# Kernel optimization log

Hardware: AMD Instinct MI355X
Metric: run time of the kernel (lower is better)

Reference implementation:

```python
import jax, jax.numpy as jnp
import numpy as np

OUT_FEATURES = 4096
IN_FEATURES = 4096
BLOCK_DIM = 16
K = 64
N_BLOCKS = OUT_FEATURES * IN_FEATURES // BLOCK_DIM  # 1,048,576


def setup_inputs() -> dict:
    key = jax.random.key(0)
    k1, k2, k3, k4, k5, k6 = jax.random.split(key, 6)
    x = jax.random.normal(k1, (8192, IN_FEATURES), dtype=jnp.float32)
    coarse_centroids = jax.random.normal(k2, (K, BLOCK_DIM), dtype=jnp.float32)
    coarse_labels = jax.random.randint(k3, (N_BLOCKS,), 0, K, dtype=jnp.int64)
    res_centroids = jax.random.normal(k4, (K, BLOCK_DIM), dtype=jnp.float32) * 0.1
    res_labels = jax.random.randint(k5, (N_BLOCKS,), 0, K, dtype=jnp.int64)
    bias = jax.random.normal(k6, (OUT_FEATURES,), dtype=jnp.float32)
    return {
        'x': x,
        'coarse_centroids': coarse_centroids,
        'coarse_labels': coarse_labels,
        'res_centroids': res_centroids,
        'res_labels': res_labels,
        'bias': bias,
    }


def _dequantize(coarse_centroids, coarse_labels, res_centroids, res_labels):
    # two-level VQ: coarse lookup + residual correction, per block of BLOCK_DIM
    blocks = coarse_centroids[coarse_labels] + res_centroids[res_labels]  # [N_BLOCKS, BLOCK_DIM]
    return blocks.reshape(OUT_FEATURES, IN_FEATURES)


def reference(x, coarse_centroids, coarse_labels, res_centroids, res_labels, bias):
    W = _dequantize(coarse_centroids, coarse_labels, res_centroids, res_labels)
    # F.linear: x @ W.T + bias
    return jnp.dot(x, W.T) + bias
```

## Files before the change

### kernel.cpp

```cpp
#include <hip/hip_runtime.h>
#include <hip/hip_bf16.h>
#include <stdint.h>

#define M_DIM 8192
#define N_DIM 4096
#define K_DIM 4096
#define BM 256
#define BN 256
#define BKQ 32
#define NT (K_DIM / BKQ)
#define THREADS 512
#define NBLOCKS_VQ (N_DIM * K_DIM / 16)

#define ATILE_B 16384
#define BOFF    65536
#define SMEM_BYTES 131072

typedef short bf16x8 __attribute__((ext_vector_type(8)));
typedef float f32x4 __attribute__((ext_vector_type(4)));
typedef unsigned short ushort_t;
typedef ushort_t ushort8 __attribute__((ext_vector_type(8)));

#define GLOBAL_AS __attribute__((address_space(1)))
#define LDS_AS __attribute__((address_space(3)))

__device__ __forceinline__ ushort_t f2bf(float f) {
  union { float f; uint32_t u; } v; v.f = f;
  uint32_t u = v.u;
  return (ushort_t)((u + 0x7FFFu + ((u >> 16) & 1u)) >> 16);
}

__global__ __launch_bounds__(256) void dequant_w(
    const float* __restrict__ cc, const int* __restrict__ cl,
    const float* __restrict__ rc, const int* __restrict__ rl,
    ushort_t* __restrict__ wout) {
  int b = blockIdx.x * 256 + threadIdx.x;
  int ci = cl[b];
  int ri = rl[b];
  const float4* c4 = (const float4*)(cc + (size_t)ci * 16);
  const float4* r4 = (const float4*)(rc + (size_t)ri * 16);
  float s[16];
#pragma unroll
  for (int p = 0; p < 4; ++p) {
    float4 a = c4[p];
    float4 r = r4[p];
    s[p * 4 + 0] = a.x + r.x;
    s[p * 4 + 1] = a.y + r.y;
    s[p * 4 + 2] = a.z + r.z;
    s[p * 4 + 3] = a.w + r.w;
  }
  ushort8 o0, o1;
#pragma unroll
  for (int j = 0; j < 8; ++j) o0[j] = f2bf(s[j]);
#pragma unroll
  for (int j = 0; j < 8; ++j) o1[j] = f2bf(s[8 + j]);
  ushort8* dst = (ushort8*)(wout + (size_t)b * 16);
  dst[0] = o0;
  dst[1] = o1;
}

__global__ __launch_bounds__(256) void cvt_x_bf16(const float* __restrict__ x,
                                                  ushort_t* __restrict__ xb) {
  size_t i = (size_t)blockIdx.x * 256 + threadIdx.x;
  const float4* p = (const float4*)x + i * 2;
  float4 a = p[0];
  float4 b = p[1];
  ushort8 o;
  o[0] = f2bf(a.x); o[1] = f2bf(a.y); o[2] = f2bf(a.z); o[3] = f2bf(a.w);
  o[4] = f2bf(b.x); o[5] = f2bf(b.y); o[6] = f2bf(b.z); o[7] = f2bf(b.w);
  ((ushort8*)xb)[i] = o;
}

__device__ __forceinline__ void stage_tile(char* smem,
    const ushort_t* gA0, const ushort_t* gB0,
    int ldsA0, int ldsB0, int tile, int buf) {
  const ushort_t* ga = gA0 + (size_t)tile * BKQ;
  const ushort_t* gb = gB0 + (size_t)tile * BKQ;
  char* la = smem + buf * ATILE_B + ldsA0;
  char* lb = smem + BOFF + buf * ATILE_B + ldsB0;
  __builtin_amdgcn_global_load_lds((const GLOBAL_AS void*)ga,
                                   (LDS_AS void*)la, 16, 0, 0);
  __builtin_amdgcn_global_load_lds((const GLOBAL_AS void*)(ga + (size_t)128 * K_DIM),
                                   (LDS_AS void*)(la + 8192), 16, 0, 0);
  __builtin_amdgcn_global_load_lds((const GLOBAL_AS void*)gb,
                                   (LDS_AS void*)lb, 16, 0, 0);
  __builtin_amdgcn_global_load_lds((const GLOBAL_AS void*)(gb + (size_t)128 * K_DIM),
                                   (LDS_AS void*)(lb + 8192), 16, 0, 0);
}

template<int VM, bool ISSUE>
__device__ __forceinline__ void kstep(char* smem,
    const ushort_t* gA0, const ushort_t* gB0, int ldsA0, int ldsB0,
    int aoff, int boff, f32x4 (&acc)[8][4], int t, int buf) {
  if constexpr (VM == 8) asm volatile("s_waitcnt vmcnt(8)" ::: "memory");
  else if constexpr (VM == 4) asm volatile("s_waitcnt vmcnt(4)" ::: "memory");
  else asm volatile("s_waitcnt vmcnt(0)" ::: "memory");
  __builtin_amdgcn_s_barrier();
  __builtin_amdgcn_sched_barrier(0);
  if constexpr (ISSUE)
    stage_tile(smem, gA0, gB0, ldsA0, ldsB0, t + 3, (buf + 3) & 3);

  const ushort_t* aB = (const ushort_t*)(smem + buf * ATILE_B) + aoff;
  const ushort_t* bB = (const ushort_t*)(smem + BOFF + buf * ATILE_B) + boff;

  bf16x8 b[4], a[4];
#pragma unroll
  for (int n = 0; n < 4; ++n) b[n] = *(const bf16x8*)(bB + n * 512);
#pragma unroll
  for (int m = 0; m < 4; ++m) a[m] = *(const bf16x8*)(aB + m * 512);
  __builtin_amdgcn_s_setprio(1);
#pragma unroll
  for (int m = 0; m < 4; ++m)
#pragma unroll
    for (int n = 0; n < 4; ++n)
      acc[m][n] = __builtin_amdgcn_mfma_f32_16x16x32_bf16(a[m], b[n], acc[m][n], 0, 0, 0);
  __builtin_amdgcn_s_setprio(0);
#pragma unroll
  for (int m = 0; m < 4; ++m) a[m] = *(const bf16x8*)(aB + 2048 + m * 512);
  __builtin_amdgcn_s_setprio(1);
#pragma unroll
  for (int m = 0; m < 4; ++m)
#pragma unroll
    for (int n = 0; n < 4; ++n)
      acc[m + 4][n] = __builtin_amdgcn_mfma_f32_16x16x32_bf16(a[m], b[n], acc[m + 4][n], 0, 0, 0);
  __builtin_amdgcn_s_setprio(0);
}

__global__ __launch_bounds__(THREADS, 2) void gemm_bf16(
    const ushort_t* __restrict__ A, const ushort_t* __restrict__ B,
    const float* __restrict__ bias, float* __restrict__ C) {
  extern __shared__ char smem[];

  const int nwg = (M_DIM / BM) * (N_DIM / BN);
  int bid = blockIdx.x;
  int swz = (bid & 7) * (nwg >> 3) + (bid >> 3);
  int bx = swz & 15;
  int by = swz >> 4;
  const int tileM = by * BM;
  const int tileN = bx * BN;

  const int tid = threadIdx.x;
  const int lane = tid & 63;
  const int wave = tid >> 6;
  const int wr = wave >> 2;
  const int wc = wave & 3;

  int srow = tid >> 2;
  int slot = tid & 3;
  int scol = ((slot ^ (srow & 3)) << 3);
  const ushort_t* gA0 = A + (size_t)(tileM + srow) * K_DIM + scol;
  const ushort_t* gB0 = B + (size_t)(tileN + srow) * K_DIM + scol;
  const int ldsA0 = wave << 10;
  const int ldsB0 = wave << 10;

  const int lrow = lane & 15;
  const int g8 = (lane >> 4) << 3;
  const int ksw = g8 ^ ((lrow & 3) << 3);
  const int aoff = (wr * 128 + lrow) * BKQ + ksw;
  const int boff = (wc * 64 + lrow) * BKQ + ksw;

  f32x4 acc[8][4];
#pragma unroll
  for (int m = 0; m < 8; ++m)
#pragma unroll
    for (int n = 0; n < 4; ++n) acc[m][n] = (f32x4)0.0f;

  stage_tile(smem, gA0, gB0, ldsA0, ldsB0, 0, 0);
  stage_tile(smem, gA0, gB0, ldsA0, ldsB0, 1, 1);
  stage_tile(smem, gA0, gB0, ldsA0, ldsB0, 2, 2);

  for (int tb = 0; tb < 31; ++tb) {
    int t = tb << 2;
    kstep<8, true>(smem, gA0, gB0, ldsA0, ldsB0, aoff, boff, acc, t + 0, 0);
    kstep<8, true>(smem, gA0, gB0, ldsA0, ldsB0, aoff, boff, acc, t + 1, 1);
    kstep<8, true>(smem, gA0, gB0, ldsA0, ldsB0, aoff, boff, acc, t + 2, 2);
    kstep<8, true>(smem, gA0, gB0, ldsA0, ldsB0, aoff, boff, acc, t + 3, 3);
  }
  kstep<8, true >(smem, gA0, gB0, ldsA0, ldsB0, aoff, boff, acc, 124, 0);
  kstep<8, false>(smem, gA0, gB0, ldsA0, ldsB0, aoff, boff, acc, 125, 1);
  kstep<4, false>(smem, gA0, gB0, ldsA0, ldsB0, aoff, boff, acc, 126, 2);
  kstep<0, false>(smem, gA0, gB0, ldsA0, ldsB0, aoff, boff, acc, 127, 3);

  const int orow = tileM + wr * 128 + ((lane >> 4) << 2);
  const int ocol0 = tileN + wc * 64 + lrow;
  float bv[4];
#pragma unroll
  for (int n = 0; n < 4; ++n) bv[n] = bias[ocol0 + n * 16];
#pragma unroll
  for (int m = 0; m < 8; ++m) {
#pragma unroll
    for (int n = 0; n < 4; ++n) {
      size_t base = (size_t)(orow + m * 16) * N_DIM + (ocol0 + n * 16);
#pragma unroll
      for (int r = 0; r < 4; ++r)
        C[base + (size_t)r * N_DIM] = acc[m][n][r] + bv[n];
    }
  }
}

extern "C" void kernel_launch(void* const* d_in, const int* in_sizes, int n_in,
                              void* d_out, int out_size, void* d_ws, size_t ws_size,
                              hipStream_t stream) {
  const float* x = (const float*)d_in[0];
  const float* cc = (const float*)d_in[1];
  const int* cl = (const int*)d_in[2];
  const float* rc = (const float*)d_in[3];
  const int* rl = (const int*)d_in[4];
  const float* bias = (const float*)d_in[5];
  float* out = (float*)d_out;

  ushort_t* Wbf = (ushort_t*)d_ws;
  ushort_t* Xbf = (ushort_t*)d_ws + (size_t)N_DIM * K_DIM;

  (void)hipFuncSetAttribute((const void*)gemm_bf16,
                            hipFuncAttributeMaxDynamicSharedMemorySize, SMEM_BYTES);

  dequant_w<<<NBLOCKS_VQ / 256, 256, 0, stream>>>(cc, cl, rc, rl, Wbf);
  cvt_x_bf16<<<(int)((M_DIM * (size_t)K_DIM / 8) / 256), 256, 0, stream>>>(x, Xbf);
  gemm_bf16<<<(M_DIM / BM) * (N_DIM / BN), THREADS, SMEM_BYTES, stream>>>(Xbf, Wbf, bias, out);
}
```

Measured before the change: 284.9 us.

## Switch GEMM to BK=64 double-buffered tiles with post-compute prefetch

The GEMM main loop changes from a 4-stage ring of BK=32 tiles to 2 buffers of BK=64 tiles. Each stage loads with 8 global-to-LDS ops per thread and a new XOR swizzle. The prefetch for tile t+2 is issued after a second barrier, once compute on the current buffer is done. This halves the number of barrier rounds per K and doubles MFMA work per step, but it shortens prefetch depth and adds a barrier, so load latency may be less well hidden.

```diff
diff --git a/kernel.cpp b/kernel.cpp
--- a/kernel.cpp
+++ b/kernel.cpp
@@ -7,13 +7,13 @@
 #define K_DIM 4096
 #define BM 256
 #define BN 256
-#define BKQ 32
-#define NT (K_DIM / BKQ)
+#define BK2 64
+#define NT2 (K_DIM / BK2)
 #define THREADS 512
 #define NBLOCKS_VQ (N_DIM * K_DIM / 16)
 
-#define ATILE_B 16384
-#define BOFF    65536
+#define TILE_B 32768
+#define BBASE  65536
 #define SMEM_BYTES 131072
 
 typedef short bf16x8 __attribute__((ext_vector_type(8)));
@@ -72,58 +72,53 @@
 }
 
 __device__ __forceinline__ void stage_tile(char* smem,
-    const ushort_t* gA0, const ushort_t* gB0,
-    int ldsA0, int ldsB0, int tile, int buf) {
-  const ushort_t* ga = gA0 + (size_t)tile * BKQ;
-  const ushort_t* gb = gB0 + (size_t)tile * BKQ;
-  char* la = smem + buf * ATILE_B + ldsA0;
-  char* lb = smem + BOFF + buf * ATILE_B + ldsB0;
-  __builtin_amdgcn_global_load_lds((const GLOBAL_AS void*)ga,
-                                   (LDS_AS void*)la, 16, 0, 0);
-  __builtin_amdgcn_global_load_lds((const GLOBAL_AS void*)(ga + (size_t)128 * K_DIM),
-                                   (LDS_AS void*)(la + 8192), 16, 0, 0);
-  __builtin_amdgcn_global_load_lds((const GLOBAL_AS void*)gb,
-                                   (LDS_AS void*)lb, 16, 0, 0);
-  __builtin_amdgcn_global_load_lds((const GLOBAL_AS void*)(gb + (size_t)128 * K_DIM),
-                                   (LDS_AS void*)(lb + 8192), 16, 0, 0);
+    const ushort_t* gA0, const ushort_t* gB0, int wbase, int tile, int buf) {
+  const ushort_t* ga = gA0 + (size_t)tile * BK2;
+  const ushort_t* gb = gB0 + (size_t)tile * BK2;
+  char* la = smem + buf * TILE_B + wbase;
+  char* lb = smem + BBASE + buf * TILE_B + wbase;
+#pragma unroll
+  for (int r = 0; r < 4; ++r) {
+    __builtin_amdgcn_global_load_lds(
+        (const GLOBAL_AS void*)(ga + (size_t)(r * 64) * K_DIM),
+        (LDS_AS void*)(la + r * 8192), 16, 0, 0);
+    __builtin_amdgcn_global_load_lds(
+        (const GLOBAL_AS void*)(gb + (size_t)(r * 64) * K_DIM),
+        (LDS_AS void*)(lb + r * 8192), 16, 0, 0);
+  }
 }
 
 template<int VM, bool ISSUE>
 __device__ __forceinline__ void kstep(char* smem,
-    const ushort_t* gA0, const ushort_t* gB0, int ldsA0, int ldsB0,
-    int aoff, int boff, f32x4 (&acc)[8][4], int t, int buf) {
+    const ushort_t* gA0, const ushort_t* gB0, int wbase,
+    int aBase, int bBase, f32x4 (&acc)[8][4], int t, int buf) {
   if constexpr (VM == 8) asm volatile("s_waitcnt vmcnt(8)" ::: "memory");
-  else if constexpr (VM == 4) asm volatile("s_waitcnt vmcnt(4)" ::: "memory");
   else asm volatile("s_waitcnt vmcnt(0)" ::: "memory");
   __builtin_amdgcn_s_barrier();
   __builtin_amdgcn_sched_barrier(0);
+
+  const ushort_t* aB = (const ushort_t*)(smem + buf * TILE_B) + aBase;
+  const ushort_t* bB = (const ushort_t*)(smem + BBASE + buf * TILE_B) + bBase;
+
+#pragma unroll
+  for (int kk = 0; kk < 2; ++kk) {
+    bf16x8 b[4], a[8];
+#pragma unroll
+    for (int n = 0; n < 4; ++n) b[n] = *(const bf16x8*)(bB + kk * 32 + n * 1024);
+#pragma unroll
+    for (int m = 0; m < 8; ++m) a[m] = *(const bf16x8*)(aB + kk * 32 + m * 1024);
+    __builtin_amdgcn_s_setprio(1);
+#pragma unroll
+    for (int m = 0; m < 8; ++m)
+#pragma unroll
+      for (int n = 0; n < 4; ++n)
+        acc[m][n] = __builtin_amdgcn_mfma_f32_16x16x32_bf16(a[m], b[n], acc[m][n], 0, 0, 0);
+    __builtin_amdgcn_s_setprio(0);
+  }
+  __builtin_amdgcn_s_barrier();
+  __builtin_amdgcn_sched_barrier(0);
   if constexpr (ISSUE)
-    stage_tile(smem, gA0, gB0, ldsA0, ldsB0, t + 3, (buf + 3) & 3);
-
-  const ushort_t* aB = (const ushort_t*)(smem + buf * ATILE_B) + aoff;
-  const ushort_t* bB = (const ushort_t*)(smem + BOFF + buf * ATILE_B) + boff;
-
-  bf16x8 b[4], a[4];
-#pragma unroll
-  for (int n = 0; n < 4; ++n) b[n] = *(const bf16x8*)(bB + n * 512);
-#pragma unroll
-  for (int m = 0; m < 4; ++m) a[m] = *(const bf16x8*)(aB + m * 512);
-  __builtin_amdgcn_s_setprio(1);
-#pragma unroll
-  for (int m = 0; m < 4; ++m)
-#pragma unroll
-    for (int n = 0; n < 4; ++n)
-      acc[m][n] = __builtin_amdgcn_mfma_f32_16x16x32_bf16(a[m], b[n], acc[m][n], 0, 0, 0);
-  __builtin_amdgcn_s_setprio(0);
-#pragma unroll
-  for (int m = 0; m < 4; ++m) a[m] = *(const bf16x8*)(aB + 2048 + m * 512);
-  __builtin_amdgcn_s_setprio(1);
-#pragma unroll
-  for (int m = 0; m < 4; ++m)
-#pragma unroll
-    for (int n = 0; n < 4; ++n)
-      acc[m + 4][n] = __builtin_amdgcn_mfma_f32_16x16x32_bf16(a[m], b[n], acc[m + 4][n], 0, 0, 0);
-  __builtin_amdgcn_s_setprio(0);
+    stage_tile(smem, gA0, gB0, wbase, t + 2, buf);
 }
 
 __global__ __launch_bounds__(THREADS, 2) void gemm_bf16(
@@ -145,19 +140,18 @@
   const int wr = wave >> 2;
   const int wc = wave & 3;
 
-  int srow = tid >> 2;
-  int slot = tid & 3;
-  int scol = ((slot ^ (srow & 3)) << 3);
+  int srow = tid >> 3;
+  int slot = tid & 7;
+  int scol = ((slot ^ ((((unsigned)srow >> 2) & 1) << 1)) << 3);
   const ushort_t* gA0 = A + (size_t)(tileM + srow) * K_DIM + scol;
   const ushort_t* gB0 = B + (size_t)(tileN + srow) * K_DIM + scol;
-  const int ldsA0 = wave << 10;
-  const int ldsB0 = wave << 10;
+  const int wbase = wave << 10;
 
   const int lrow = lane & 15;
   const int g8 = (lane >> 4) << 3;
-  const int ksw = g8 ^ ((lrow & 3) << 3);
-  const int aoff = (wr * 128 + lrow) * BKQ + ksw;
-  const int boff = (wc * 64 + lrow) * BKQ + ksw;
+  const int kx = g8 ^ ((lrow & 4) << 2);
+  const int aBase = (wr * 128 + lrow) * 64 + kx;
+  const int bBase = (wc * 64 + lrow) * 64 + kx;
 
   f32x4 acc[8][4];
 #pragma unroll
@@ -165,21 +159,15 @@
 #pragma unroll
     for (int n = 0; n < 4; ++n) acc[m][n] = (f32x4)0.0f;
 
-  stage_tile(smem, gA0, gB0, ldsA0, ldsB0, 0, 0);
-  stage_tile(smem, gA0, gB0, ldsA0, ldsB0, 1, 1);
-  stage_tile(smem, gA0, gB0, ldsA0, ldsB0, 2, 2);
+  stage_tile(smem, gA0, gB0, wbase, 0, 0);
+  stage_tile(smem, gA0, gB0, wbase, 1, 1);
 
   for (int tb = 0; tb < 31; ++tb) {
-    int t = tb << 2;
-    kstep<8, true>(smem, gA0, gB0, ldsA0, ldsB0, aoff, boff, acc, t + 0, 0);
-    kstep<8, true>(smem, gA0, gB0, ldsA0, ldsB0, aoff, boff, acc, t + 1, 1);
-    kstep<8, true>(smem, gA0, gB0, ldsA0, ldsB0, aoff, boff, acc, t + 2, 2);
-    kstep<8, true>(smem, gA0, gB0, ldsA0, ldsB0, aoff, boff, acc, t + 3, 3);
-  }
-  kstep<8, true >(smem, gA0, gB0, ldsA0, ldsB0, aoff, boff, acc, 124, 0);
-  kstep<8, false>(smem, gA0, gB0, ldsA0, ldsB0, aoff, boff, acc, 125, 1);
-  kstep<4, false>(smem, gA0, gB0, ldsA0, ldsB0, aoff, boff, acc, 126, 2);
-  kstep<0, false>(smem, gA0, gB0, ldsA0, ldsB0, aoff, boff, acc, 127, 3);
+    kstep<8, true>(smem, gA0, gB0, wbase, aBase, bBase, acc, 2 * tb, 0);
+    kstep<8, true>(smem, gA0, gB0, wbase, aBase, bBase, acc, 2 * tb + 1, 1);
+  }
+  kstep<8, false>(smem, gA0, gB0, wbase, aBase, bBase, acc, 62, 0);
+  kstep<0, false>(smem, gA0, gB0, wbase, aBase, bBase, acc, 63, 1);
 
   const int orow = tileM + wr * 128 + ((lane >> 4) << 2);
   const int ocol0 = tileN + wc * 64 + lrow;
```

Result: slower. 299.4 us (+5.1%).
